# Kernel tuning notes

Hardware: AMD Instinct MI355X
Metric: run time of the kernel (lower is better)

The kernel has to match this reference:

```python
import jax, jax.numpy as jnp
import numpy as np

ARITY = 8        # children per node (< max_child_number=10, so all children used)
TREE_DEPTH = 5   # internal levels 1..5; depth=5 so GRU applies at every internal node
DIM = 384        # cgf_input_dim == GRU input == GRU hidden (unidirectional, n_layers=1)
VOCAB = 32000


def gru_seq(xs, h0, w_ih, w_hh, b_ih, b_hh):
    # xs: [S, N, D] sequence-major, h0: [N, D]. torch nn.GRU gate order: r, z, n.
    def step(h, x_t):
        gi = x_t @ w_ih.T + b_ih            # [N, 3D]
        gh = h @ w_hh.T + b_hh              # [N, 3D]
        i_r, i_z, i_n = jnp.split(gi, 3, axis=-1)
        h_r, h_z, h_n = jnp.split(gh, 3, axis=-1)
        r = jax.nn.sigmoid(i_r + h_r)
        z = jax.nn.sigmoid(i_z + h_z)
        n = jnp.tanh(i_n + r * h_n)
        h_new = (1.0 - z) * n + z * h
        return h_new, h_new
    h_last, outs = jax.lax.scan(step, h0, xs)
    return outs, h_last                      # [S, N, D], [N, D]


def setup_inputs() -> dict:
    key = jax.random.key(0)
    k1, k2, k3, k4, k5, k6 = jax.random.split(key, 6)
    n_leaves = ARITY ** TREE_DEPTH
    s = 1.0 / np.sqrt(DIM)
    return {
        "leaf_tokens": jax.random.randint(k1, (n_leaves,), 0, VOCAB, dtype=jnp.int32),
        "embed_table": jax.random.normal(k2, (VOCAB, DIM), jnp.float32),
        "w_ih": jax.random.uniform(k3, (3 * DIM, DIM), jnp.float32, -s, s),
        "w_hh": jax.random.uniform(k4, (3 * DIM, DIM), jnp.float32, -s, s),
        "b_ih": jax.random.uniform(k5, (3 * DIM,), jnp.float32, -s, s),
        "b_hh": jax.random.uniform(k6, (3 * DIM,), jnp.float32, -s, s),
    }


def reference(leaf_tokens, embed_table, w_ih, w_hh, b_ih, b_hh):
    # Leaves: embedding-dict lookup -> x=[1,1,D] per leaf; h = zeros.
    x = embed_table[leaf_tokens]             # [A^T, D]
    h = jnp.zeros_like(x)                    # leaf hidden states are zeros
    # Level-synchronous post-order: process deepest internal level first.
    for level in range(TREE_DEPTH, 0, -1):
        n_parents = ARITY ** (level - 1)
        # Children are consumed from last to first (loop i = len-1 .. 0), so
        # the GRU sequence is the REVERSED child order.
        xs = x.reshape(n_parents, ARITY, DIM)[:, ::-1, :].transpose(1, 0, 2)  # [A, P, D]
        h0 = h.reshape(n_parents, ARITY, DIM).mean(axis=1)                     # mean of child hiddens
        outs, h = gru_seq(xs, h0, w_ih, w_hh, b_ih, b_hh)
        x = outs.mean(axis=0)                # mean over the child sequence -> node output [P, D]
    # Root (layer=1) returns res = out of shape [1,1,D]
    return x.reshape(1, 1, DIM)
```

## Files before the change

kernel.cpp:

```cpp
#include <hip/hip_runtime.h>
#include <hip/hip_bf16.h>
#include <stdint.h>

typedef float f32x4 __attribute__((ext_vector_type(4)));
typedef short bf16x8 __attribute__((ext_vector_type(8)));

__device__ __forceinline__ ushort to_bf16(float f) {
    union { float f; uint32_t u; } v; v.f = f;
    uint32_t u = v.u;
    return (ushort)((u + 0x7fffu + ((u >> 16) & 1u)) >> 16);
}
__device__ __forceinline__ float sigmoid_(float x) { return 1.0f / (1.0f + __expf(-x)); }
__device__ __forceinline__ float tanh_(float x)    { return 1.0f - 2.0f / (__expf(2.0f * x) + 1.0f); }

__global__ void prep_w(const float* __restrict__ w_ih, const float* __restrict__ w_hh,
                       ushort* __restrict__ wswz) {
    int tid = blockIdx.x * blockDim.x + threadIdx.x;
    if (tid >= 1152 * 96) return;
    int g  = tid / 96;
    int k  = (tid % 96) * 8;
    int kc = k >> 5;
    int q  = (k >> 3) & 3;
    int tile = g >> 4;
    int lane = q * 16 + (g & 15);
    ushort* dst = wswz + ((size_t)(tile * 24 + kc) * 64 + lane) * 8;
    const float* src = (k < 384) ? (w_ih + (size_t)g * 384 + k)
                                 : (w_hh + (size_t)g * 384 + (k - 384));
#pragma unroll
    for (int j = 0; j < 8; ++j) dst[j] = to_bf16(src[j]);
}

__global__ void embed_gather(const int* __restrict__ tok, const float* __restrict__ table,
                             ushort* __restrict__ xleaf, int n_leaves) {
    int tid = blockIdx.x * blockDim.x + threadIdx.x;
    if (tid >= n_leaves * 48) return;
    int leaf = tid / 48, i = tid % 48;
    const float* src = table + (size_t)tok[leaf] * 384 + i * 8;
    bf16x8 v;
#pragma unroll
    for (int j = 0; j < 8; ++j) v[j] = (short)to_bf16(src[j]);
    *(bf16x8*)(xleaf + (size_t)leaf * 384 + i * 8) = v;
}

__global__ void init_h(const float* __restrict__ Hc, float* __restrict__ HT0,
                       ushort* __restrict__ HB0, int P) {
    int tid = blockIdx.x * blockDim.x + threadIdx.x;
    if (tid >= P * 384) return;
    int p = tid / 384, d = tid % 384;
    float h0 = 0.0f;
#pragma unroll
    for (int c = 0; c < 8; ++c) h0 += Hc[((size_t)p * 8 + c) * 384 + d];
    h0 *= 0.125f;
    HT0[tid] = h0; HB0[tid] = to_bf16(h0);
}

__global__ __launch_bounds__(256, 4)
void gru_step(const ushort* __restrict__ Xc, ushort* __restrict__ HB,
              float* __restrict__ HT, const ushort* __restrict__ W,
              const float* __restrict__ b_ih, const float* __restrict__ b_hh,
              ushort* __restrict__ Xo, float* __restrict__ fout,
              int P, int t, int flags) {
    const int wave = threadIdx.x >> 6, lane = threadIdx.x & 63;
    const int quad = lane >> 4, col = lane & 15;
    const int m0 = (blockIdx.x * 4 + wave) * 32;
    if (m0 >= P) return;
    const int ds = blockIdx.y;
    const bool hzero = (flags & 1) != 0, last = (flags & 2) != 0;
    const bool do2 = (m0 + 16) < P;
    const int child = 7 - t;
    const size_t N = (size_t)P * 384;

    const ushort* HBprev = HB + (size_t)t * N;
    ushort*       HBcur  = HB + (size_t)(t + 1) * N;
    const float*  HTprev = HT + (size_t)t * N;
    float*        HTcur  = HT + (size_t)(t + 1) * N;

    const int par0 = m0 + col, par1 = m0 + 16 + col;
    const bool av0 = par0 < P, av1 = par1 < P;
    const ushort* xr0 = Xc + ((size_t)par0 * 8 + child) * 384 + quad * 8;
    const ushort* xr1 = Xc + ((size_t)par1 * 8 + child) * 384 + quad * 8;
    const ushort* hr0 = HBprev + (size_t)par0 * 384 + quad * 8;
    const ushort* hr1 = HBprev + (size_t)par1 * 384 + quad * 8;
    const ushort* Wl = W + (size_t)lane * 8;
    const size_t oR = (size_t)ds * 12288;
    const size_t oZ = (size_t)(24 + ds) * 12288;
    const size_t oN = (size_t)(48 + ds) * 12288;

    const int d = ds * 16 + col;
    const float br = b_ih[d] + b_hh[d];
    const float bz = b_ih[384 + d] + b_hh[384 + d];
    const float bi = b_ih[768 + d], bh = b_hh[768 + d];
    float hp[2][4];
#pragma unroll
    for (int mt = 0; mt < 2; ++mt)
#pragma unroll
        for (int r = 0; r < 4; ++r) {
            int m = m0 + mt * 16 + quad * 4 + r;
            hp[mt][r] = (!hzero && m < P) ? HTprev[(size_t)m * 384 + d] : 0.0f;
        }

    f32x4 z4 = (f32x4){0.f, 0.f, 0.f, 0.f};
    f32x4 accr0 = z4, accz0 = z4, accn10 = z4, accn20 = z4;
    f32x4 accr1 = z4, accz1 = z4, accn11 = z4, accn21 = z4;
    const bf16x8 zf = (bf16x8){0, 0, 0, 0, 0, 0, 0, 0};

#pragma unroll
    for (int kc = 0; kc < 12; ++kc) {
        bf16x8 a0 = zf, a1 = zf;
        if (av0) a0 = *(const bf16x8*)(xr0 + kc * 32);
        if (do2 && av1) a1 = *(const bf16x8*)(xr1 + kc * 32);
        const size_t kb = (size_t)kc * 512;
        bf16x8 bR = *(const bf16x8*)(Wl + oR + kb);
        bf16x8 bZ = *(const bf16x8*)(Wl + oZ + kb);
        bf16x8 bN = *(const bf16x8*)(Wl + oN + kb);
        accr0 = __builtin_amdgcn_mfma_f32_16x16x32_bf16(a0, bR, accr0, 0, 0, 0);
        accz0 = __builtin_amdgcn_mfma_f32_16x16x32_bf16(a0, bZ, accz0, 0, 0, 0);
        accn10 = __builtin_amdgcn_mfma_f32_16x16x32_bf16(a0, bN, accn10, 0, 0, 0);
        if (do2) {
            accr1 = __builtin_amdgcn_mfma_f32_16x16x32_bf16(a1, bR, accr1, 0, 0, 0);
            accz1 = __builtin_amdgcn_mfma_f32_16x16x32_bf16(a1, bZ, accz1, 0, 0, 0);
            accn11 = __builtin_amdgcn_mfma_f32_16x16x32_bf16(a1, bN, accn11, 0, 0, 0);
        }
    }
    if (!hzero) {
#pragma unroll
        for (int kc = 0; kc < 12; ++kc) {
            bf16x8 a0 = zf, a1 = zf;
            if (av0) a0 = *(const bf16x8*)(hr0 + kc * 32);
            if (do2 && av1) a1 = *(const bf16x8*)(hr1 + kc * 32);
            const size_t kb = (size_t)(12 + kc) * 512;
            bf16x8 bR = *(const bf16x8*)(Wl + oR + kb);
            bf16x8 bZ = *(const bf16x8*)(Wl + oZ + kb);
            bf16x8 bN = *(const bf16x8*)(Wl + oN + kb);
            accr0 = __builtin_amdgcn_mfma_f32_16x16x32_bf16(a0, bR, accr0, 0, 0, 0);
            accz0 = __builtin_amdgcn_mfma_f32_16x16x32_bf16(a0, bZ, accz0, 0, 0, 0);
            accn20 = __builtin_amdgcn_mfma_f32_16x16x32_bf16(a0, bN, accn20, 0, 0, 0);
            if (do2) {
                accr1 = __builtin_amdgcn_mfma_f32_16x16x32_bf16(a1, bR, accr1, 0, 0, 0);
                accz1 = __builtin_amdgcn_mfma_f32_16x16x32_bf16(a1, bZ, accz1, 0, 0, 0);
                accn21 = __builtin_amdgcn_mfma_f32_16x16x32_bf16(a1, bN, accn21, 0, 0, 0);
            }
        }
    }

#pragma unroll
    for (int mt = 0; mt < 2; ++mt) {
        if (mt && !do2) break;
        const f32x4 ar  = mt ? accr1  : accr0;
        const f32x4 az  = mt ? accz1  : accz0;
        const f32x4 an1 = mt ? accn11 : accn10;
        const f32x4 an2 = mt ? accn21 : accn20;
#pragma unroll
        for (int r = 0; r < 4; ++r) {
            const int m = m0 + mt * 16 + quad * 4 + r;
            if (m < P) {
                const size_t idx = (size_t)m * 384 + d;
                float rv = sigmoid_(ar[r] + br);
                float zv = sigmoid_(az[r] + bz);
                float nv = tanh_(an1[r] + bi + rv * (an2[r] + bh));
                float hn = (1.0f - zv) * nv + zv * hp[mt][r];
                HTcur[idx] = hn;
                HBcur[idx] = to_bf16(hn);
                if (last) {
                    float xs = hn + hp[mt][r];
#pragma unroll
                    for (int s = 1; s <= 6; ++s) xs += HT[(size_t)s * N + idx];
                    float xo = xs * 0.125f;
                    Xo[idx] = to_bf16(xo);
                    if (fout != nullptr && m == 0) fout[d] = xo;
                }
            }
        }
    }
}

extern "C" void kernel_launch(void* const* d_in, const int* in_sizes, int n_in,
                              void* d_out, int out_size, void* d_ws, size_t ws_size,
                              hipStream_t stream) {
    const int*   tok   = (const int*)d_in[0];
    const float* table = (const float*)d_in[1];
    const float* w_ih  = (const float*)d_in[2];
    const float* w_hh  = (const float*)d_in[3];
    const float* b_ih  = (const float*)d_in[4];
    const float* b_hh  = (const float*)d_in[5];
    float* out = (float*)d_out;

    char* ws = (char*)d_ws;
    size_t off = 0;
    auto alloc = [&](size_t bytes) -> void* {
        void* p = ws + off;
        off = (off + bytes + 255) & ~(size_t)255;
        return p;
    };
    ushort* wswz = (ushort*)alloc((size_t)1152 * 768 * 2);
    ushort* XA   = (ushort*)alloc((size_t)32768 * 384 * 2);

    struct Lvl { ushort *HB, *Xo; float *HT; int P; };
    auto mk = [&](int P) -> Lvl {
        Lvl l; l.P = P;
        size_t N = (size_t)P * 384;
        l.HB = (ushort*)alloc(9 * N * 2);
        l.HT = (float*) alloc(9 * N * 4);
        l.Xo = (ushort*)alloc(N * 2);
        return l;
    };
    Lvl L5 = mk(4096), L4 = mk(512), L3 = mk(64), L2 = mk(8), L1 = mk(1);

    prep_w<<<(1152 * 96 + 255) / 256, 256, 0, stream>>>(w_ih, w_hh, wswz);
    embed_gather<<<(32768 * 48 + 255) / 256, 256, 0, stream>>>(tok, table, XA, 32768);

    auto run_level = [&](const ushort* Xc, const float* Hc_child, Lvl& L,
                         float* fout, bool leaf) {
        int P = L.P;
        if (!leaf)
            init_h<<<(P * 384 + 255) / 256, 256, 0, stream>>>(Hc_child, L.HT, L.HB, P);
        int gx = (P + 127) / 128;
        dim3 grid(gx, 24);
        for (int t = 0; t < 8; ++t) {
            int flags = ((leaf && t == 0) ? 1 : 0) | (t == 7 ? 2 : 0);
            gru_step<<<grid, 256, 0, stream>>>(Xc, L.HB, L.HT, wswz, b_ih, b_hh,
                                               L.Xo, (t == 7) ? fout : nullptr,
                                               P, t, flags);
        }
    };

    run_level(XA, nullptr, L5, nullptr, true);
    run_level(L5.Xo, L5.HT + (size_t)8 * 4096 * 384, L4, nullptr, false);
    run_level(L4.Xo, L4.HT + (size_t)8 * 512 * 384,  L3, nullptr, false);
    run_level(L3.Xo, L3.HT + (size_t)8 * 64 * 384,   L2, nullptr, false);
    run_level(L2.Xo, L2.HT + (size_t)8 * 8 * 384,    L1, out,     false);
}
```

Before: 659.1 us.

## Fuse next-level h0 mean into last GRU step and widen per-wave output tile

Removes the separate init_h kernel by computing each next-level parent's mean hidden state in the final timestep's epilogue, using a cross-lane shuffle to combine the two quads that cover one parent's 8 children. The final step also stops writing the unused ninth hidden-state slot, which shrinks the per-level buffers to eight slots. Each wave now computes two 16-column output tiles, halving grid.y from 24 to 12, so every A-fragment load feeds twice as many MFMAs. The trade-off is more accumulator registers, so launch bounds are lowered to 3 waves-per-SIMD occupancy, and gx is rounded up to a multiple of 8.

```diff
diff --git a/kernel.cpp b/kernel.cpp
--- a/kernel.cpp
+++ b/kernel.cpp
@@ -42,136 +42,159 @@
     *(bf16x8*)(xleaf + (size_t)leaf * 384 + i * 8) = v;
 }
 
-__global__ void init_h(const float* __restrict__ Hc, float* __restrict__ HT0,
-                       ushort* __restrict__ HB0, int P) {
-    int tid = blockIdx.x * blockDim.x + threadIdx.x;
-    if (tid >= P * 384) return;
-    int p = tid / 384, d = tid % 384;
-    float h0 = 0.0f;
-#pragma unroll
-    for (int c = 0; c < 8; ++c) h0 += Hc[((size_t)p * 8 + c) * 384 + d];
-    h0 *= 0.125f;
-    HT0[tid] = h0; HB0[tid] = to_bf16(h0);
-}
-
-__global__ __launch_bounds__(256, 4)
+#define MFMA(a, b, c) __builtin_amdgcn_mfma_f32_16x16x32_bf16((a), (b), (c), 0, 0, 0)
+
+__global__ __launch_bounds__(256, 3)
 void gru_step(const ushort* __restrict__ Xc, ushort* __restrict__ HB,
               float* __restrict__ HT, const ushort* __restrict__ W,
               const float* __restrict__ b_ih, const float* __restrict__ b_hh,
-              ushort* __restrict__ Xo, float* __restrict__ fout,
-              int P, int t, int flags) {
+              ushort* __restrict__ Xo, float* __restrict__ HTn,
+              ushort* __restrict__ HBn, float* __restrict__ fout,
+              int P, int Pn, int t, int flags) {
     const int wave = threadIdx.x >> 6, lane = threadIdx.x & 63;
     const int quad = lane >> 4, col = lane & 15;
     const int m0 = (blockIdx.x * 4 + wave) * 32;
     if (m0 >= P) return;
     const int ds = blockIdx.y;
-    const bool hzero = (flags & 1) != 0, last = (flags & 2) != 0;
+    const bool hz = (flags & 1) != 0, last = (flags & 2) != 0;
     const bool do2 = (m0 + 16) < P;
     const int child = 7 - t;
     const size_t N = (size_t)P * 384;
 
-    const ushort* HBprev = HB + (size_t)t * N;
-    ushort*       HBcur  = HB + (size_t)(t + 1) * N;
-    const float*  HTprev = HT + (size_t)t * N;
-    float*        HTcur  = HT + (size_t)(t + 1) * N;
+    const ushort* HBp = HB + (size_t)t * N;
+    const float*  HTp = HT + (size_t)t * N;
 
     const int par0 = m0 + col, par1 = m0 + 16 + col;
     const bool av0 = par0 < P, av1 = par1 < P;
     const ushort* xr0 = Xc + ((size_t)par0 * 8 + child) * 384 + quad * 8;
     const ushort* xr1 = Xc + ((size_t)par1 * 8 + child) * 384 + quad * 8;
-    const ushort* hr0 = HBprev + (size_t)par0 * 384 + quad * 8;
-    const ushort* hr1 = HBprev + (size_t)par1 * 384 + quad * 8;
+    const ushort* hr0 = HBp + (size_t)par0 * 384 + quad * 8;
+    const ushort* hr1 = HBp + (size_t)par1 * 384 + quad * 8;
     const ushort* Wl = W + (size_t)lane * 8;
-    const size_t oR = (size_t)ds * 12288;
-    const size_t oZ = (size_t)(24 + ds) * 12288;
-    const size_t oN = (size_t)(48 + ds) * 12288;
-
-    const int d = ds * 16 + col;
-    const float br = b_ih[d] + b_hh[d];
-    const float bz = b_ih[384 + d] + b_hh[384 + d];
-    const float bi = b_ih[768 + d], bh = b_hh[768 + d];
-    float hp[2][4];
-#pragma unroll
-    for (int mt = 0; mt < 2; ++mt)
-#pragma unroll
-        for (int r = 0; r < 4; ++r) {
-            int m = m0 + mt * 16 + quad * 4 + r;
-            hp[mt][r] = (!hzero && m < P) ? HTprev[(size_t)m * 384 + d] : 0.0f;
-        }
-
-    f32x4 z4 = (f32x4){0.f, 0.f, 0.f, 0.f};
-    f32x4 accr0 = z4, accz0 = z4, accn10 = z4, accn20 = z4;
-    f32x4 accr1 = z4, accz1 = z4, accn11 = z4, accn21 = z4;
+    size_t oR[2], oZ[2], oN[2];
+#pragma unroll
+    for (int j = 0; j < 2; ++j) {
+        oR[j] = (size_t)(2 * ds + j) * 12288;
+        oZ[j] = (size_t)(24 + 2 * ds + j) * 12288;
+        oN[j] = (size_t)(48 + 2 * ds + j) * 12288;
+    }
+
+    int dj[2]; float br[2], bz[2], bi[2], bh[2];
+#pragma unroll
+    for (int j = 0; j < 2; ++j) {
+        dj[j] = ds * 32 + j * 16 + col;
+        br[j] = b_ih[dj[j]] + b_hh[dj[j]];
+        bz[j] = b_ih[384 + dj[j]] + b_hh[384 + dj[j]];
+        bi[j] = b_ih[768 + dj[j]];
+        bh[j] = b_hh[768 + dj[j]];
+    }
+    float hp[2][2][4];
+#pragma unroll
+    for (int j = 0; j < 2; ++j)
+#pragma unroll
+        for (int mt = 0; mt < 2; ++mt)
+#pragma unroll
+            for (int r = 0; r < 4; ++r) {
+                const int m = m0 + mt * 16 + quad * 4 + r;
+                hp[j][mt][r] = (!hz && m < P) ? HTp[(size_t)m * 384 + dj[j]] : 0.0f;
+            }
+
+    const f32x4 z4 = (f32x4){0.f, 0.f, 0.f, 0.f};
     const bf16x8 zf = (bf16x8){0, 0, 0, 0, 0, 0, 0, 0};
+    f32x4 ar[2][2], az[2][2], an1[2][2], an2[2][2];
+#pragma unroll
+    for (int j = 0; j < 2; ++j)
+#pragma unroll
+        for (int mt = 0; mt < 2; ++mt) {
+            ar[j][mt] = z4; az[j][mt] = z4; an1[j][mt] = z4; an2[j][mt] = z4;
+        }
 
 #pragma unroll
     for (int kc = 0; kc < 12; ++kc) {
-        bf16x8 a0 = zf, a1 = zf;
-        if (av0) a0 = *(const bf16x8*)(xr0 + kc * 32);
-        if (do2 && av1) a1 = *(const bf16x8*)(xr1 + kc * 32);
+        bf16x8 a0 = av0 ? *(const bf16x8*)(xr0 + kc * 32) : zf;
+        bf16x8 a1 = (do2 && av1) ? *(const bf16x8*)(xr1 + kc * 32) : zf;
         const size_t kb = (size_t)kc * 512;
-        bf16x8 bR = *(const bf16x8*)(Wl + oR + kb);
-        bf16x8 bZ = *(const bf16x8*)(Wl + oZ + kb);
-        bf16x8 bN = *(const bf16x8*)(Wl + oN + kb);
-        accr0 = __builtin_amdgcn_mfma_f32_16x16x32_bf16(a0, bR, accr0, 0, 0, 0);
-        accz0 = __builtin_amdgcn_mfma_f32_16x16x32_bf16(a0, bZ, accz0, 0, 0, 0);
-        accn10 = __builtin_amdgcn_mfma_f32_16x16x32_bf16(a0, bN, accn10, 0, 0, 0);
-        if (do2) {
-            accr1 = __builtin_amdgcn_mfma_f32_16x16x32_bf16(a1, bR, accr1, 0, 0, 0);
-            accz1 = __builtin_amdgcn_mfma_f32_16x16x32_bf16(a1, bZ, accz1, 0, 0, 0);
-            accn11 = __builtin_amdgcn_mfma_f32_16x16x32_bf16(a1, bN, accn11, 0, 0, 0);
-        }
-    }
-    if (!hzero) {
+#pragma unroll
+        for (int j = 0; j < 2; ++j) {
+            const bf16x8 bR = *(const bf16x8*)(Wl + oR[j] + kb);
+            const bf16x8 bZ = *(const bf16x8*)(Wl + oZ[j] + kb);
+            const bf16x8 bN = *(const bf16x8*)(Wl + oN[j] + kb);
+            ar[j][0]  = MFMA(a0, bR, ar[j][0]);
+            az[j][0]  = MFMA(a0, bZ, az[j][0]);
+            an1[j][0] = MFMA(a0, bN, an1[j][0]);
+            if (do2) {
+                ar[j][1]  = MFMA(a1, bR, ar[j][1]);
+                az[j][1]  = MFMA(a1, bZ, az[j][1]);
+                an1[j][1] = MFMA(a1, bN, an1[j][1]);
+            }
+        }
+    }
+    if (!hz) {
 #pragma unroll
         for (int kc = 0; kc < 12; ++kc) {
-            bf16x8 a0 = zf, a1 = zf;
-            if (av0) a0 = *(const bf16x8*)(hr0 + kc * 32);
-            if (do2 && av1) a1 = *(const bf16x8*)(hr1 + kc * 32);
+            bf16x8 a0 = av0 ? *(const bf16x8*)(hr0 + kc * 32) : zf;
+            bf16x8 a1 = (do2 && av1) ? *(const bf16x8*)(hr1 + kc * 32) : zf;
             const size_t kb = (size_t)(12 + kc) * 512;
-            bf16x8 bR = *(const bf16x8*)(Wl + oR + kb);
-            bf16x8 bZ = *(const bf16x8*)(Wl + oZ + kb);
-            bf16x8 bN = *(const bf16x8*)(Wl + oN + kb);
-            accr0 = __builtin_amdgcn_mfma_f32_16x16x32_bf16(a0, bR, accr0, 0, 0, 0);
-            accz0 = __builtin_amdgcn_mfma_f32_16x16x32_bf16(a0, bZ, accz0, 0, 0, 0);
-            accn20 = __builtin_amdgcn_mfma_f32_16x16x32_bf16(a0, bN, accn20, 0, 0, 0);
-            if (do2) {
-                accr1 = __builtin_amdgcn_mfma_f32_16x16x32_bf16(a1, bR, accr1, 0, 0, 0);
-                accz1 = __builtin_amdgcn_mfma_f32_16x16x32_bf16(a1, bZ, accz1, 0, 0, 0);
-                accn21 = __builtin_amdgcn_mfma_f32_16x16x32_bf16(a1, bN, accn21, 0, 0, 0);
-            }
-        }
-    }
-
-#pragma unroll
-    for (int mt = 0; mt < 2; ++mt) {
-        if (mt && !do2) break;
-        const f32x4 ar  = mt ? accr1  : accr0;
-        const f32x4 az  = mt ? accz1  : accz0;
-        const f32x4 an1 = mt ? accn11 : accn10;
-        const f32x4 an2 = mt ? accn21 : accn20;
-#pragma unroll
-        for (int r = 0; r < 4; ++r) {
-            const int m = m0 + mt * 16 + quad * 4 + r;
-            if (m < P) {
-                const size_t idx = (size_t)m * 384 + d;
-                float rv = sigmoid_(ar[r] + br);
-                float zv = sigmoid_(az[r] + bz);
-                float nv = tanh_(an1[r] + bi + rv * (an2[r] + bh));
-                float hn = (1.0f - zv) * nv + zv * hp[mt][r];
-                HTcur[idx] = hn;
-                HBcur[idx] = to_bf16(hn);
-                if (last) {
-                    float xs = hn + hp[mt][r];
-#pragma unroll
-                    for (int s = 1; s <= 6; ++s) xs += HT[(size_t)s * N + idx];
-                    float xo = xs * 0.125f;
-                    Xo[idx] = to_bf16(xo);
-                    if (fout != nullptr && m == 0) fout[d] = xo;
+#pragma unroll
+            for (int j = 0; j < 2; ++j) {
+                const bf16x8 bR = *(const bf16x8*)(Wl + oR[j] + kb);
+                const bf16x8 bZ = *(const bf16x8*)(Wl + oZ[j] + kb);
+                const bf16x8 bN = *(const bf16x8*)(Wl + oN[j] + kb);
+                ar[j][0]  = MFMA(a0, bR, ar[j][0]);
+                az[j][0]  = MFMA(a0, bZ, az[j][0]);
+                an2[j][0] = MFMA(a0, bN, an2[j][0]);
+                if (do2) {
+                    ar[j][1]  = MFMA(a1, bR, ar[j][1]);
+                    az[j][1]  = MFMA(a1, bZ, az[j][1]);
+                    an2[j][1] = MFMA(a1, bN, an2[j][1]);
                 }
             }
         }
     }
+
+#pragma unroll
+    for (int j = 0; j < 2; ++j)
+#pragma unroll
+        for (int mt = 0; mt < 2; ++mt) {
+            if (mt && !do2) break;
+            float s4 = 0.0f;
+#pragma unroll
+            for (int r = 0; r < 4; ++r) {
+                const int m = m0 + mt * 16 + quad * 4 + r;
+                if (m < P) {
+                    const size_t idx = (size_t)m * 384 + dj[j];
+                    const float rv = sigmoid_(ar[j][mt][r] + br[j]);
+                    const float zv = sigmoid_(az[j][mt][r] + bz[j]);
+                    const float nv = tanh_(an1[j][mt][r] + bi[j]
+                                           + rv * (an2[j][mt][r] + bh[j]));
+                    const float hn = (1.0f - zv) * nv + zv * hp[j][mt][r];
+                    s4 += hn;
+                    if (!last) {
+                        HT[(size_t)(t + 1) * N + idx] = hn;
+                        HB[(size_t)(t + 1) * N + idx] = to_bf16(hn);
+                    } else {
+                        float xs = hn + hp[j][mt][r];
+#pragma unroll
+                        for (int s = 1; s <= 6; ++s) xs += HT[(size_t)s * N + idx];
+                        const float xo = xs * 0.125f;
+                        Xo[idx] = to_bf16(xo);
+                        if (fout != nullptr && m == 0) fout[dj[j]] = xo;
+                    }
+                }
+            }
+            if (last && HTn != nullptr) {
+                const float o = __shfl_xor(s4, 16, 64);
+                if ((quad & 1) == 0) {
+                    const int ti = (m0 >> 4) + mt;
+                    const int pnode = 2 * ti + (quad >> 1);
+                    if (pnode < Pn) {
+                        const float h0 = (s4 + o) * 0.125f;
+                        HTn[(size_t)pnode * 384 + dj[j]] = h0;
+                        HBn[(size_t)pnode * 384 + dj[j]] = to_bf16(h0);
+                    }
+                }
+            }
+        }
 }
 
 extern "C" void kernel_launch(void* const* d_in, const int* in_sizes, int n_in,
@@ -199,34 +222,31 @@
     auto mk = [&](int P) -> Lvl {
         Lvl l; l.P = P;
         size_t N = (size_t)P * 384;
-        l.HB = (ushort*)alloc(9 * N * 2);
-        l.HT = (float*) alloc(9 * N * 4);
+        l.HT = (float*) alloc(8 * N * 4);
+        l.HB = (ushort*)alloc(8 * N * 2);
         l.Xo = (ushort*)alloc(N * 2);
         return l;
     };
-    Lvl L5 = mk(4096), L4 = mk(512), L3 = mk(64), L2 = mk(8), L1 = mk(1);
+    Lvl L[5] = {mk(4096), mk(512), mk(64), mk(8), mk(1)};
 
     prep_w<<<(1152 * 96 + 255) / 256, 256, 0, stream>>>(w_ih, w_hh, wswz);
     embed_gather<<<(32768 * 48 + 255) / 256, 256, 0, stream>>>(tok, table, XA, 32768);
 
-    auto run_level = [&](const ushort* Xc, const float* Hc_child, Lvl& L,
-                         float* fout, bool leaf) {
-        int P = L.P;
-        if (!leaf)
-            init_h<<<(P * 384 + 255) / 256, 256, 0, stream>>>(Hc_child, L.HT, L.HB, P);
+    for (int lv = 0; lv < 5; ++lv) {
+        const ushort* Xc = (lv == 0) ? XA : L[lv - 1].Xo;
+        int P = L[lv].P;
+        int Pn = (lv < 4) ? L[lv + 1].P : 0;
+        float*  HTn = (lv < 4) ? L[lv + 1].HT : nullptr;
+        ushort* HBn = (lv < 4) ? L[lv + 1].HB : nullptr;
         int gx = (P + 127) / 128;
-        dim3 grid(gx, 24);
+        gx = (gx + 7) & ~7;
+        dim3 grid(gx, 12);
         for (int t = 0; t < 8; ++t) {
-            int flags = ((leaf && t == 0) ? 1 : 0) | (t == 7 ? 2 : 0);
-            gru_step<<<grid, 256, 0, stream>>>(Xc, L.HB, L.HT, wswz, b_ih, b_hh,
-                                               L.Xo, (t == 7) ? fout : nullptr,
-                                               P, t, flags);
-        }
-    };
-
-    run_level(XA, nullptr, L5, nullptr, true);
-    run_level(L5.Xo, L5.HT + (size_t)8 * 4096 * 384, L4, nullptr, false);
-    run_level(L4.Xo, L4.HT + (size_t)8 * 512 * 384,  L3, nullptr, false);
-    run_level(L3.Xo, L3.HT + (size_t)8 * 64 * 384,   L2, nullptr, false);
-    run_level(L2.Xo, L2.HT + (size_t)8 * 8 * 384,    L1, out,     false);
-}
+            int flags = ((lv == 0 && t == 0) ? 1 : 0) | (t == 7 ? 2 : 0);
+            gru_step<<<grid, 256, 0, stream>>>(
+                Xc, L[lv].HB, L[lv].HT, wswz, b_ih, b_hh, L[lv].Xo,
+                (t == 7) ? HTn : nullptr, HBn, (lv == 4 && t == 7) ? out : nullptr,
+                P, Pn, t, flags);
+        }
+    }
+}
```

Result: slower. 932.1 us (+41.4%).
